# Performance work log

Measured on AMD Instinct MI355X. Metric: run time of the kernel, lower is better.

Reference implementation:

```python
import jax, jax.numpy as jnp
import numpy as np

CHUNK = 4096
DECAY = 0.99
EPS = 1e-5


def setup_inputs() -> dict:
    key = jax.random.key(0)
    k1, k2, k3, k4 = jax.random.split(key, 4)
    z = jax.random.normal(k1, (32, 64, 32, 32), dtype=jnp.float32)
    codebook = jax.random.normal(k2, (8192, 64), dtype=jnp.float32)
    cluster_size = jax.random.uniform(k3, (8192,), dtype=jnp.float32)
    embed_avg = jax.random.normal(k4, (8192, 64), dtype=jnp.float32)
    return {"z": z, "codebook": codebook, "cluster_size": cluster_size, "embed_avg": embed_avg}


def _nearest_indices(vectors, codebook):
    """Chunked fp32 squared-L2 nearest-neighbor search (matches _nearest_indices)."""
    cb = codebook.astype(jnp.float32)
    c2 = jnp.sum(cb * cb, axis=1)  # [K]

    def chunk_fn(chunk):
        v = chunk.astype(jnp.float32)  # [CHUNK, D]
        d = jnp.sum(v * v, axis=1, keepdims=True) + c2[None, :] - 2.0 * (v @ cb.T)
        return jnp.argmin(d, axis=1)

    n, d = vectors.shape  # n divisible by CHUNK by construction
    chunks = vectors.reshape(n // CHUNK, CHUNK, d)
    return jax.lax.map(chunk_fn, chunks).reshape(-1)


def reference(z, codebook, cluster_size, embed_avg):
    B, C, H, W = z.shape
    K = codebook.shape[0]
    # [B,C,H,W] -> [N,C]
    vectors = jnp.transpose(z, (0, 2, 3, 1)).reshape(-1, C)
    N = vectors.shape[0]

    indices = _nearest_indices(vectors, codebook)  # [N] int
    quantized = jnp.transpose(codebook[indices].reshape(B, H, W, C), (0, 3, 1, 2))

    # commitment loss (codebook learned via EMA, so only encoder side differentiable)
    vq_loss = jnp.mean((jax.lax.stop_gradient(quantized) - z) ** 2)
    # straight-through estimator
    quantized_st = z + jax.lax.stop_gradient(quantized - z)

    # code usage statistics
    counts = jax.ops.segment_sum(jnp.ones((N,), jnp.float32), indices, num_segments=K)
    avg_probs = counts / N
    perplexity = jnp.exp(-jnp.sum(avg_probs * jnp.log(avg_probs + 1e-10)))
    active_codes = jnp.sum(counts > 0).astype(jnp.int32)

    # EMA update (scatter-add accumulation + Laplace-smoothed normalization)
    sums = jax.ops.segment_sum(vectors.astype(jnp.float32), indices, num_segments=K)
    new_cluster_size = DECAY * cluster_size + (1.0 - DECAY) * counts
    new_embed_avg = DECAY * embed_avg + (1.0 - DECAY) * sums
    n_total = jnp.sum(new_cluster_size)
    smoothed = (new_cluster_size + EPS) / (n_total + K * EPS) * n_total
    new_codebook = new_embed_avg / smoothed[:, None]

    return (quantized_st, indices, vq_loss, perplexity, active_codes,
            new_codebook, new_cluster_size, new_embed_avg)
```

## Files before the change

### kernel.cpp

```cpp
#include <hip/hip_runtime.h>
#include <math.h>

typedef unsigned short u16;
typedef unsigned int u32;
typedef unsigned long long u64;
typedef __attribute__((ext_vector_type(8))) short short8;
typedef __attribute__((ext_vector_type(4))) float f32x4;

#define NVEC   32768
#define DIMV   64
#define KC     8192
#define NKCH   4
#define CHK    2048
#define HW     1024
#define BPLANE 65536

#define OFF_Q    0
#define OFF_IDX  2097152
#define OFF_LOSS 2129920
#define OFF_PPL  2129921
#define OFF_ACT  2129922
#define OFF_NCB  2129923
#define OFF_NCS  2654211
#define OFF_NEA  2662403

#define WS_COUNTS 0
#define WS_SCAL   8192
#define WS_C2     8200
#define WS_MINP   16400
#define WS_OFFS   81936
#define WS_PERM   90128
#define WS_CBH    122896
#define WS_CBM    385040
#define WS_CBL    647184

__device__ __forceinline__ u16 f2bf(float x) {
    u32 u = __float_as_uint(x);
    u += 0x7fffu + ((u >> 16) & 1u);
    return (u16)(u >> 16);
}
__device__ __forceinline__ float bf2f(u16 h) {
    return __uint_as_float(((u32)h) << 16);
}
__device__ __forceinline__ u32 fmono(float f) {
    u32 b = __float_as_uint(f);
    return (b & 0x80000000u) ? ~b : (b | 0x80000000u);
}

__global__ __launch_bounds__(256) void cbsplit_kernel(const float* __restrict__ cb,
                                                      u16* __restrict__ cbh,
                                                      u16* __restrict__ cbm,
                                                      u16* __restrict__ cbl,
                                                      float* __restrict__ c2) {
    const int t = threadIdx.x;
    const int k = blockIdx.x * 4 + (t >> 6);
    const int d = t & 63;
    const int idx = k * DIMV + d;
    float x = cb[idx];
    u16 hb = f2bf(x);  float fh = bf2f(hb);
    float r1 = x - fh; u16 mb = f2bf(r1); float fm = bf2f(mb);
    float r2 = r1 - fm; u16 lb = f2bf(r2);
    cbh[idx] = hb; cbm[idx] = mb; cbl[idx] = lb;
    float s = x * x;
    for (int off = 32; off > 0; off >>= 1) s += __shfl_down(s, off, 64);
    if (d == 0) c2[k] = s;
}

#define NN_COMPUTE(Bh0, Bh1, Bm0, Bm1, Bl0, Bl1, CM, NTI)                          \
    _Pragma("unroll")                                                               \
    for (int i = 0; i < 4; ++i) {                                                   \
        f32x4 acc = {CM, CM, CM, CM};                                               \
        acc = __builtin_amdgcn_mfma_f32_16x16x32_bf16(A[i][0][0], Bh0, acc, 0, 0, 0);\
        acc = __builtin_amdgcn_mfma_f32_16x16x32_bf16(A[i][0][1], Bh1, acc, 0, 0, 0);\
        acc = __builtin_amdgcn_mfma_f32_16x16x32_bf16(A[i][1][0], Bh0, acc, 0, 0, 0);\
        acc = __builtin_amdgcn_mfma_f32_16x16x32_bf16(A[i][1][1], Bh1, acc, 0, 0, 0);\
        acc = __builtin_amdgcn_mfma_f32_16x16x32_bf16(A[i][0][0], Bm0, acc, 0, 0, 0);\
        acc = __builtin_amdgcn_mfma_f32_16x16x32_bf16(A[i][0][1], Bm1, acc, 0, 0, 0);\
        acc = __builtin_amdgcn_mfma_f32_16x16x32_bf16(A[i][1][0], Bm0, acc, 0, 0, 0);\
        acc = __builtin_amdgcn_mfma_f32_16x16x32_bf16(A[i][1][1], Bm1, acc, 0, 0, 0);\
        acc = __builtin_amdgcn_mfma_f32_16x16x32_bf16(A[i][2][0], Bh0, acc, 0, 0, 0);\
        acc = __builtin_amdgcn_mfma_f32_16x16x32_bf16(A[i][2][1], Bh1, acc, 0, 0, 0);\
        acc = __builtin_amdgcn_mfma_f32_16x16x32_bf16(A[i][0][0], Bl0, acc, 0, 0, 0);\
        acc = __builtin_amdgcn_mfma_f32_16x16x32_bf16(A[i][0][1], Bl1, acc, 0, 0, 0);\
        _Pragma("unroll")                                                           \
        for (int r = 0; r < 4; ++r) {                                               \
            float a = acc[r];                                                       \
            if (a > bestv[i][r]) { bestv[i][r] = a; bestn[i][r] = (NTI); }          \
        }                                                                           \
    }

#define NN_LOAD(Dh0, Dh1, Dm0, Dm1, Dl0, Dl1, DCM, NTI) {                          \
        const int to_ = (NTI) * 16 * DIMV;                                          \
        DCM = -0.5f * pc2[(NTI) * 16];                                              \
        Dh0 = *(const short8*)(ph + to_);                                           \
        Dh1 = *(const short8*)(ph + to_ + 32);                                      \
        Dm0 = *(const short8*)(pm + to_);                                           \
        Dm1 = *(const short8*)(pm + to_ + 32);                                      \
        Dl0 = *(const short8*)(pl + to_);                                           \
        Dl1 = *(const short8*)(pl + to_ + 32);                                      \
    }

__global__ __launch_bounds__(256, 2) void nn_kernel(const float* __restrict__ z,
                                                    const u16* __restrict__ cbh,
                                                    const u16* __restrict__ cbm,
                                                    const u16* __restrict__ cbl,
                                                    const float* __restrict__ c2,
                                                    u64* __restrict__ minp) {
    const int l  = threadIdx.x & 63;
    const int w  = threadIdx.x >> 6;
    const int vg = blockIdx.x;
    const int kc = blockIdx.y;
    const int m0 = vg * 256 + w * 64;
    const int lr = l & 15;
    const int lg = l >> 4;

    short8 A[4][3][2];
#pragma unroll
    for (int i = 0; i < 4; ++i) {
        const int vec = m0 + i * 16 + lr;
        const float* zp = z + (size_t)(vec >> 10) * BPLANE + (vec & 1023);
#pragma unroll
        for (int s = 0; s < 2; ++s) {
            short8 ah, am, al;
#pragma unroll
            for (int e = 0; e < 8; ++e) {
                const int k = s * 32 + lg * 8 + e;
                float x = zp[k * HW];
                u16 hb = f2bf(x);   float fh = bf2f(hb);
                float r1 = x - fh;  u16 mb = f2bf(r1); float fm = bf2f(mb);
                float r2 = r1 - fm; u16 lb = f2bf(r2);
                ah[e] = (short)hb; am[e] = (short)mb; al[e] = (short)lb;
            }
            A[i][0][s] = ah; A[i][1][s] = am; A[i][2][s] = al;
        }
    }

    float bestv[4][4];
    int   bestn[4][4];
#pragma unroll
    for (int i = 0; i < 4; ++i)
#pragma unroll
        for (int r = 0; r < 4; ++r) { bestv[i][r] = -3.4e38f; bestn[i][r] = 0; }

    const int code_base = kc * CHK;
    const u16* ph = cbh + (size_t)(code_base + lr) * DIMV + lg * 8;
    const u16* pm = cbm + (size_t)(code_base + lr) * DIMV + lg * 8;
    const u16* pl = cbl + (size_t)(code_base + lr) * DIMV + lg * 8;
    const float* pc2 = c2 + code_base + lr;

    const int NT = CHK / 16;

    short8 P_h0, P_h1, P_m0, P_m1, P_l0, P_l1;
    short8 Q_h0, Q_h1, Q_m0, Q_m1, Q_l0, Q_l1;
    float cm0, cm1;

    NN_LOAD(P_h0, P_h1, P_m0, P_m1, P_l0, P_l1, cm0, 0)

    for (int nt = 0; nt < NT; nt += 2) {
        NN_LOAD(Q_h0, Q_h1, Q_m0, Q_m1, Q_l0, Q_l1, cm1, nt + 1)
        NN_COMPUTE(P_h0, P_h1, P_m0, P_m1, P_l0, P_l1, cm0, nt)
        if (nt + 2 < NT) {
            NN_LOAD(P_h0, P_h1, P_m0, P_m1, P_l0, P_l1, cm0, nt + 2)
        }
        NN_COMPUTE(Q_h0, Q_h1, Q_m0, Q_m1, Q_l0, Q_l1, cm1, nt + 1)
    }

#pragma unroll
    for (int i = 0; i < 4; ++i)
#pragma unroll
        for (int r = 0; r < 4; ++r) {
            float v = bestv[i][r];
            int idx = bestn[i][r] * 16 + lr;
#pragma unroll
            for (int mk = 1; mk < 16; mk <<= 1) {
                float ov = __shfl_xor(v, mk, 64);
                int   oi = __shfl_xor(idx, mk, 64);
                if (ov > v || (ov == v && oi < idx)) { v = ov; idx = oi; }
            }
            if (lr == 0) {
                const int vec = m0 + i * 16 + lg * 4 + r;
                const u64 pack = ((u64)fmono(-v) << 32) | (u32)(code_base + idx);
                atomicMin(&minp[vec], pack);
            }
        }
}

__global__ __launch_bounds__(256) void gather_kernel(const float* __restrict__ z,
                                                     const float* __restrict__ cb,
                                                     const u64* __restrict__ minp,
                                                     float* __restrict__ out,
                                                     float* __restrict__ counts,
                                                     float* __restrict__ scal) {
    const int n = blockIdx.x * 256 + threadIdx.x;
    const int bi = (int)(u32)(minp[n] & 0xFFFFFFFFu);
    out[OFF_IDX + n] = (float)bi;
    atomicAdd(&counts[bi], 1.0f);

    const int b = n >> 10, h = n & 1023;
    const float* zp = z + (size_t)b * BPLANE + h;
    const float* cp = cb + (size_t)bi * DIMV;
    float* qp = out + OFF_Q + (size_t)b * BPLANE + h;
    float acc = 0.f;
#pragma unroll
    for (int c = 0; c < DIMV; ++c) {
        float zv = zp[c * HW];
        float q = cp[c];
        float df = q - zv;
        acc = fmaf(df, df, acc);
        qp[c * HW] = zv + df;
    }
    for (int off = 32; off > 0; off >>= 1) acc += __shfl_down(acc, off, 64);
    __shared__ float red[4];
    if ((threadIdx.x & 63) == 0) red[threadIdx.x >> 6] = acc;
    __syncthreads();
    if (threadIdx.x == 0) atomicAdd(&scal[0], (red[0] + red[1]) + (red[2] + red[3]));
}

__global__ __launch_bounds__(256) void prefix_kernel(const float* __restrict__ counts,
                                                     int* __restrict__ offs) {
    __shared__ int part[256];
    const int t = threadIdx.x;
    const int base = t * 32;
    int loc[32];
    int s = 0;
#pragma unroll
    for (int j = 0; j < 32; ++j) { loc[j] = s; s += (int)counts[base + j]; }
    part[t] = s;
    __syncthreads();
    for (int off = 1; off < 256; off <<= 1) {
        int v = (t >= off) ? part[t - off] : 0;
        __syncthreads();
        part[t] += v;
        __syncthreads();
    }
    const int excl = part[t] - s;
#pragma unroll
    for (int j = 0; j < 32; ++j) offs[base + j] = excl + loc[j];
}

__global__ __launch_bounds__(256) void scatter_kernel(const float* __restrict__ outIdx,
                                                      int* __restrict__ offs,
                                                      int* __restrict__ perm) {
    const int n = blockIdx.x * 256 + threadIdx.x;
    const int bi = (int)outIdx[n];
    const int pos = atomicAdd(&offs[bi], 1);
    perm[pos] = n;
}

__global__ __launch_bounds__(256) void segsum_kernel(const float* __restrict__ z,
                                                     const float* __restrict__ counts,
                                                     const int* __restrict__ offs,
                                                     const int* __restrict__ perm,
                                                     float* __restrict__ sums) {
    const int w = threadIdx.x >> 6;
    const int c = threadIdx.x & 63;
    const int k = blockIdx.x * 4 + w;
    const int end = offs[k];
    const int cnt = (int)counts[k];
    float s = 0.f;
    for (int m = end - cnt; m < end; ++m) {
        const int n = perm[m];
        s += z[(size_t)(n >> 10) * BPLANE + (size_t)c * HW + (n & 1023)];
    }
    sums[k * DIMV + c] = s;
}

__global__ __launch_bounds__(256) void stats_kernel(const float* __restrict__ cs,
                                                    const float* __restrict__ counts,
                                                    float* __restrict__ out,
                                                    float* __restrict__ scal) {
    const int k = blockIdx.x * 256 + threadIdx.x;
    const float cnt = counts[k];
    float ncs = 0.99f * cs[k] + 0.01f * cnt;
    out[OFF_NCS + k] = ncs;
    float p = cnt * (1.0f / 32768.0f);
    float pl = p * logf(p + 1e-10f);
    float act = (cnt > 0.f) ? 1.f : 0.f;
    for (int off = 32; off > 0; off >>= 1) {
        ncs += __shfl_down(ncs, off, 64);
        pl  += __shfl_down(pl,  off, 64);
        act += __shfl_down(act, off, 64);
    }
    __shared__ float r0[4], r1[4], r2[4];
    const int w = threadIdx.x >> 6;
    if ((threadIdx.x & 63) == 0) { r0[w] = ncs; r1[w] = pl; r2[w] = act; }
    __syncthreads();
    if (threadIdx.x == 0) {
        atomicAdd(&scal[1], (r0[0] + r0[1]) + (r0[2] + r0[3]));
        atomicAdd(&scal[2], (r1[0] + r1[1]) + (r1[2] + r1[3]));
        atomicAdd(&scal[3], (r2[0] + r2[1]) + (r2[2] + r2[3]));
    }
}

__global__ __launch_bounds__(256) void final_kernel(const float* __restrict__ ea,
                                                    const float* __restrict__ sums,
                                                    float* __restrict__ out,
                                                    const float* __restrict__ scal) {
    const int i = blockIdx.x * 256 + threadIdx.x;
    const float nea = 0.99f * ea[i] + 0.01f * sums[i];
    out[OFF_NEA + i] = nea;
    const float nt = scal[1];
    const int k = i >> 6;
    const float ncs = out[OFF_NCS + k];
    const float sm = ((ncs + 1e-5f) / (nt + 0.08192f)) * nt;
    out[OFF_NCB + i] = nea / sm;
    if (i == 0) {
        out[OFF_LOSS] = scal[0] * (1.0f / 2097152.0f);
        out[OFF_PPL]  = expf(-scal[2]);
        out[OFF_ACT]  = scal[3];
    }
}

extern "C" void kernel_launch(void* const* d_in, const int* in_sizes, int n_in,
                              void* d_out, int out_size, void* d_ws, size_t ws_size,
                              hipStream_t stream) {
    const float* z  = (const float*)d_in[0];
    const float* cb = (const float*)d_in[1];
    const float* cs = (const float*)d_in[2];
    const float* ea = (const float*)d_in[3];
    float* out = (float*)d_out;
    float* ws  = (float*)d_ws;

    float* counts = ws + WS_COUNTS;
    float* scal   = ws + WS_SCAL;
    float* c2     = ws + WS_C2;
    u64*   minp   = (u64*)(ws + WS_MINP);
    int*   offs   = (int*)(ws + WS_OFFS);
    int*   perm   = (int*)(ws + WS_PERM);
    u16*   cbh    = (u16*)(ws + WS_CBH);
    u16*   cbm    = (u16*)(ws + WS_CBM);
    u16*   cbl    = (u16*)(ws + WS_CBL);
    float* sums   = ws + WS_CBH;

    hipMemsetAsync(ws, 0, 8200 * 4, stream);
    hipMemsetAsync(minp, 0xFF, NVEC * 8, stream);
    cbsplit_kernel<<<KC / 4, 256, 0, stream>>>(cb, cbh, cbm, cbl, c2);
    nn_kernel<<<dim3(128, NKCH), 256, 0, stream>>>(z, cbh, cbm, cbl, c2, minp);
    gather_kernel<<<NVEC / 256, 256, 0, stream>>>(z, cb, minp, out, counts, scal);
    prefix_kernel<<<1, 256, 0, stream>>>(counts, offs);
    scatter_kernel<<<NVEC / 256, 256, 0, stream>>>(out + OFF_IDX, offs, perm);
    segsum_kernel<<<KC / 4, 256, 0, stream>>>(z, counts, offs, perm, sums);
    stats_kernel<<<KC / 256, 256, 0, stream>>>(cs, counts, out, scal);
    final_kernel<<<524288 / 256, 256, 0, stream>>>(ea, sums, out, scal);
}
```

Before: 295.6 us.

## Stage codebook tiles into LDS via direct global-to-LDS loads with fragment layout

The codebook split kernel now writes the hi/mid/lo bf16 parts into a single interleaved buffer laid out as per-tile MFMA B fragments. The NN kernel stages two 16-code tiles per step into double-buffered shared memory using global_load_lds, so the four waves in a block share one copy instead of each wave loading the codebook from global memory itself. This trades redundant global/L2 traffic for LDS reads plus a block barrier on every step.

```diff
diff --git a/kernel.cpp b/kernel.cpp
--- a/kernel.cpp
+++ b/kernel.cpp
@@ -14,6 +14,7 @@
 #define CHK    2048
 #define HW     1024
 #define BPLANE 65536
+#define NSTEP  (CHK / 32)
 
 #define OFF_Q    0
 #define OFF_IDX  2097152
@@ -30,9 +31,7 @@
 #define WS_MINP   16400
 #define WS_OFFS   81936
 #define WS_PERM   90128
-#define WS_CBH    122896
-#define WS_CBM    385040
-#define WS_CBL    647184
+#define WS_CBF    122896
 
 __device__ __forceinline__ u16 f2bf(float x) {
     u32 u = __float_as_uint(x);
@@ -48,9 +47,7 @@
 }
 
 __global__ __launch_bounds__(256) void cbsplit_kernel(const float* __restrict__ cb,
-                                                      u16* __restrict__ cbh,
-                                                      u16* __restrict__ cbm,
-                                                      u16* __restrict__ cbl,
+                                                      u16* __restrict__ cbf,
                                                       float* __restrict__ c2) {
     const int t = threadIdx.x;
     const int k = blockIdx.x * 4 + (t >> 6);
@@ -60,7 +57,14 @@
     u16 hb = f2bf(x);  float fh = bf2f(hb);
     float r1 = x - fh; u16 mb = f2bf(r1); float fm = bf2f(mb);
     float r2 = r1 - fm; u16 lb = f2bf(r2);
-    cbh[idx] = hb; cbm[idx] = mb; cbl[idx] = lb;
+    const int ti = k >> 4, row = k & 15;
+    const int half = d >> 5;
+    const int cg = (d >> 3) & 3;
+    const int le = row + cg * 16;
+    u16* base = cbf + (size_t)ti * 3072 + le * 8 + (d & 7);
+    base[(0 + half) * 512] = hb;
+    base[(2 + half) * 512] = mb;
+    base[(4 + half) * 512] = lb;
     float s = x * x;
     for (int off = 32; off > 0; off >>= 1) s += __shfl_down(s, off, 64);
     if (d == 0) c2[k] = s;
@@ -89,28 +93,27 @@
         }                                                                           \
     }
 
-#define NN_LOAD(Dh0, Dh1, Dm0, Dm1, Dl0, Dl1, DCM, NTI) {                          \
-        const int to_ = (NTI) * 16 * DIMV;                                          \
-        DCM = -0.5f * pc2[(NTI) * 16];                                              \
-        Dh0 = *(const short8*)(ph + to_);                                           \
-        Dh1 = *(const short8*)(ph + to_ + 32);                                      \
-        Dm0 = *(const short8*)(pm + to_);                                           \
-        Dm1 = *(const short8*)(pm + to_ + 32);                                      \
-        Dl0 = *(const short8*)(pl + to_);                                           \
-        Dl1 = *(const short8*)(pl + to_ + 32);                                      \
+#define STAGE(B, ST)                                                                \
+    _Pragma("unroll")                                                               \
+    for (int j = 0; j < 3; ++j) {                                                   \
+        const u16* gs = pcbf + (size_t)(ST) * 6144 + j * 2048 + tl * 8;             \
+        u16* ld = &ldsb[B][j * 2048 + wv * 512];                                    \
+        __builtin_amdgcn_global_load_lds(                                           \
+            (const __attribute__((address_space(1))) void*)gs,                      \
+            (__attribute__((address_space(3))) void*)ld, 16, 0, 0);                 \
     }
 
 __global__ __launch_bounds__(256, 2) void nn_kernel(const float* __restrict__ z,
-                                                    const u16* __restrict__ cbh,
-                                                    const u16* __restrict__ cbm,
-                                                    const u16* __restrict__ cbl,
+                                                    const u16* __restrict__ cbf,
                                                     const float* __restrict__ c2,
                                                     u64* __restrict__ minp) {
-    const int l  = threadIdx.x & 63;
-    const int w  = threadIdx.x >> 6;
+    __shared__ __align__(16) u16 ldsb[2][6144];
+    const int tl = threadIdx.x;
+    const int l  = tl & 63;
+    const int wv = tl >> 6;
     const int vg = blockIdx.x;
     const int kc = blockIdx.y;
-    const int m0 = vg * 256 + w * 64;
+    const int m0 = vg * 256 + wv * 64;
     const int lr = l & 15;
     const int lg = l >> 4;
 
@@ -143,26 +146,39 @@
         for (int r = 0; r < 4; ++r) { bestv[i][r] = -3.4e38f; bestn[i][r] = 0; }
 
     const int code_base = kc * CHK;
-    const u16* ph = cbh + (size_t)(code_base + lr) * DIMV + lg * 8;
-    const u16* pm = cbm + (size_t)(code_base + lr) * DIMV + lg * 8;
-    const u16* pl = cbl + (size_t)(code_base + lr) * DIMV + lg * 8;
     const float* pc2 = c2 + code_base + lr;
-
-    const int NT = CHK / 16;
-
-    short8 P_h0, P_h1, P_m0, P_m1, P_l0, P_l1;
-    short8 Q_h0, Q_h1, Q_m0, Q_m1, Q_l0, Q_l1;
-    float cm0, cm1;
-
-    NN_LOAD(P_h0, P_h1, P_m0, P_m1, P_l0, P_l1, cm0, 0)
-
-    for (int nt = 0; nt < NT; nt += 2) {
-        NN_LOAD(Q_h0, Q_h1, Q_m0, Q_m1, Q_l0, Q_l1, cm1, nt + 1)
-        NN_COMPUTE(P_h0, P_h1, P_m0, P_m1, P_l0, P_l1, cm0, nt)
-        if (nt + 2 < NT) {
-            NN_LOAD(P_h0, P_h1, P_m0, P_m1, P_l0, P_l1, cm0, nt + 2)
+    const u16* pcbf = cbf + (size_t)kc * (CHK / 16) * 3072;
+
+    STAGE(0, 0)
+    __syncthreads();
+
+    for (int st = 0; st < NSTEP; ++st) {
+        const int b = st & 1;
+        const float cmA = -0.5f * pc2[(st * 2) * 16];
+        const float cmB = -0.5f * pc2[(st * 2 + 1) * 16];
+        if (st + 1 < NSTEP) { STAGE(b ^ 1, st + 1) }
+
+        const u16* baseA = &ldsb[b][l * 8];
+        {
+            short8 h0 = *(const short8*)(baseA);
+            short8 h1 = *(const short8*)(baseA + 512);
+            short8 m0f = *(const short8*)(baseA + 1024);
+            short8 m1f = *(const short8*)(baseA + 1536);
+            short8 l0f = *(const short8*)(baseA + 2048);
+            short8 l1f = *(const short8*)(baseA + 2560);
+            NN_COMPUTE(h0, h1, m0f, m1f, l0f, l1f, cmA, st * 2)
         }
-        NN_COMPUTE(Q_h0, Q_h1, Q_m0, Q_m1, Q_l0, Q_l1, cm1, nt + 1)
+        {
+            const u16* baseB = baseA + 3072;
+            short8 h0 = *(const short8*)(baseB);
+            short8 h1 = *(const short8*)(baseB + 512);
+            short8 m0f = *(const short8*)(baseB + 1024);
+            short8 m1f = *(const short8*)(baseB + 1536);
+            short8 l0f = *(const short8*)(baseB + 2048);
+            short8 l1f = *(const short8*)(baseB + 2560);
+            NN_COMPUTE(h0, h1, m0f, m1f, l0f, l1f, cmB, st * 2 + 1)
+        }
+        __syncthreads();
     }
 
 #pragma unroll
@@ -327,15 +343,13 @@
     u64*   minp   = (u64*)(ws + WS_MINP);
     int*   offs   = (int*)(ws + WS_OFFS);
     int*   perm   = (int*)(ws + WS_PERM);
-    u16*   cbh    = (u16*)(ws + WS_CBH);
-    u16*   cbm    = (u16*)(ws + WS_CBM);
-    u16*   cbl    = (u16*)(ws + WS_CBL);
-    float* sums   = ws + WS_CBH;
+    u16*   cbf    = (u16*)(ws + WS_CBF);
+    float* sums   = ws + WS_CBF;
 
     hipMemsetAsync(ws, 0, 8200 * 4, stream);
     hipMemsetAsync(minp, 0xFF, NVEC * 8, stream);
-    cbsplit_kernel<<<KC / 4, 256, 0, stream>>>(cb, cbh, cbm, cbl, c2);
-    nn_kernel<<<dim3(128, NKCH), 256, 0, stream>>>(z, cbh, cbm, cbl, c2, minp);
+    cbsplit_kernel<<<KC / 4, 256, 0, stream>>>(cb, cbf, c2);
+    nn_kernel<<<dim3(128, NKCH), 256, 0, stream>>>(z, cbf, c2, minp);
     gather_kernel<<<NVEC / 256, 256, 0, stream>>>(z, cb, minp, out, counts, scal);
     prefix_kernel<<<1, 256, 0, stream>>>(counts, offs);
     scatter_kernel<<<NVEC / 256, 256, 0, stream>>>(out + OFF_IDX, offs, perm);
```

Result: faster. 258.0 us (-12.7%).
